# Kernel tuning notes

Measured on AMD Instinct MI355X. Metric: run time of the kernel, lower is better.

The kernel has to match this reference:

```python
import jax, jax.numpy as jnp
import numpy as np

N_NODES = 100000
N_EDGES = 1600000
IN_DIM = 128
HID = 128
NUM_LAYERS = 10
NUM_CLASSES = 2
NUM_GRAPHS = 64


def setup_inputs() -> dict:
    key = jax.random.key(0)
    ks = jax.random.split(key, 16)
    x = jax.random.normal(ks[0], (N_NODES, IN_DIM), dtype=jnp.float32)
    # edges with no self loops (GIN_Conv calls remove_self_loops)
    src = jax.random.randint(ks[1], (N_EDGES,), 0, N_NODES)
    off = jax.random.randint(ks[2], (N_EDGES,), 1, N_NODES)
    dst = (src + off) % N_NODES
    edge_index = jnp.stack([src, dst]).astype(jnp.int64)
    batch = jnp.sort(jax.random.randint(ks[3], (N_NODES,), 0, NUM_GRAPHS)).astype(jnp.int64)
    s = 1.0 / np.sqrt(HID)
    eps = jnp.zeros((NUM_LAYERS,), dtype=jnp.float32)
    W1 = jax.random.normal(ks[4], (NUM_LAYERS, IN_DIM, HID), dtype=jnp.float32) * s
    b1 = jnp.zeros((NUM_LAYERS, HID), dtype=jnp.float32)
    W2 = jax.random.normal(ks[5], (NUM_LAYERS, HID, HID), dtype=jnp.float32) * s
    b2 = jnp.zeros((NUM_LAYERS, HID), dtype=jnp.float32)
    Wc1 = jax.random.normal(ks[6], (HID, HID), dtype=jnp.float32) * s
    bc1 = jnp.zeros((HID,), dtype=jnp.float32)
    Wc2 = jax.random.normal(ks[7], (HID, NUM_CLASSES), dtype=jnp.float32) * s
    bc2 = jnp.zeros((NUM_CLASSES,), dtype=jnp.float32)
    return {"x": x, "edge_index": edge_index, "batch": batch, "eps": eps,
            "W1": W1, "b1": b1, "W2": W2, "b2": b2,
            "Wc1": Wc1, "bc1": bc1, "Wc2": Wc2, "bc2": bc2}


def _gin_block(x, src, dst, eps_i, W1_i, b1_i, W2_i, b2_i, mlp_residual):
    # gather-scatter add aggregation: aggr[v] = sum_{(u->v)} x[u]
    aggr = jax.ops.segment_sum(x[src], dst, num_segments=N_NODES)
    h = (1.0 + eps_i) * x + aggr
    out = jnp.dot(jax.nn.relu(jnp.dot(h, W1_i) + b1_i), W2_i) + b2_i
    if mlp_residual:  # MLP internal residual (layers i > 0)
        out = out + h
    out = jax.nn.relu(out)  # ResidualGNNBlock: Identity norm, relu, Identity dropout
    out = out + x  # block residual (dims match: in_dim == hidden)
    return out


def reference(x, edge_index, batch, eps, W1, b1, W2, b2, Wc1, bc1, Wc2, bc2):
    src, dst = edge_index[0], edge_index[1]
    for i in range(NUM_LAYERS):
        x = _gin_block(x, src, dst, eps[i], W1[i], b1[i], W2[i], b2[i], mlp_residual=(i > 0))
    # global_mean_pool
    sums = jax.ops.segment_sum(x, batch, num_segments=NUM_GRAPHS)
    cnts = jax.ops.segment_sum(jnp.ones((x.shape[0], 1), x.dtype), batch, num_segments=NUM_GRAPHS)
    pooled = sums / jnp.maximum(cnts, 1.0)
    # classifier MLP (dropout inactive in eval)
    logits = jnp.dot(jax.nn.relu(jnp.dot(pooled, Wc1) + bc1), Wc2) + bc2
    return logits
```

## Files before the change

kernel.cpp:

```cpp
#include <hip/hip_runtime.h>


#define N_NODES 100000
#define N_EDGES 1600000
#define HID 128
#define NUM_LAYERS 10
#define NUM_GRAPHS 64
#define SCAN_BLOCKS ((N_NODES + 255) / 256)
#define ROWS 32
#define IDX_CAP 1024


__global__ __launch_bounds__(256) void count_deg_kernel(const int* __restrict__ dst,
                                                        int* __restrict__ deg, int E) {
  int e = blockIdx.x * 256 + threadIdx.x;
  if (e < E) atomicAdd(&deg[dst[e]], 1);
}

__global__ __launch_bounds__(256) void block_sum_kernel(const int* __restrict__ deg,
                                                        int* __restrict__ psum, int n) {
  __shared__ int sd[256];
  int i = blockIdx.x * 256 + threadIdx.x;
  sd[threadIdx.x] = (i < n) ? deg[i] : 0;
  __syncthreads();
  for (int off = 128; off > 0; off >>= 1) {
    if (threadIdx.x < off) sd[threadIdx.x] += sd[threadIdx.x + off];
    __syncthreads();
  }
  if (threadIdx.x == 0) psum[blockIdx.x] = sd[0];
}

__global__ __launch_bounds__(512) void scan_partials_kernel(const int* __restrict__ psum,
                                                            int* __restrict__ poff, int nb) {
  __shared__ int sd[512];
  int i = threadIdx.x;
  int v = (i < nb) ? psum[i] : 0;
  sd[i] = v;
  __syncthreads();
  for (int off = 1; off < 512; off <<= 1) {
    int t = (i >= off) ? sd[i - off] : 0;
    __syncthreads();
    sd[i] += t;
    __syncthreads();
  }
  if (i < nb) poff[i] = sd[i] - v;
}

__global__ __launch_bounds__(256) void write_rs_kernel(const int* __restrict__ deg,
                                                       const int* __restrict__ poff,
                                                       int* __restrict__ rs,
                                                       int* __restrict__ cur, int n) {
  __shared__ int sd[256];
  int i = blockIdx.x * 256 + threadIdx.x;
  int v = (i < n) ? deg[i] : 0;
  sd[threadIdx.x] = v;
  __syncthreads();
  for (int off = 1; off < 256; off <<= 1) {
    int t = (threadIdx.x >= off) ? sd[threadIdx.x - off] : 0;
    __syncthreads();
    sd[threadIdx.x] += t;
    __syncthreads();
  }
  if (i < n) {
    int incl = poff[blockIdx.x] + sd[threadIdx.x];
    rs[i + 1] = incl;
    cur[i] = incl - v;
  }
  if (i == 0) rs[0] = 0;
}

__global__ __launch_bounds__(256) void fill_csr_kernel(const int* __restrict__ src,
                                                       const int* __restrict__ dst,
                                                       int* __restrict__ cur,
                                                       int* __restrict__ csr, int E) {
  int e = blockIdx.x * 256 + threadIdx.x;
  if (e < E) {
    int p = atomicAdd(&cur[dst[e]], 1);
    csr[p] = src[e];
  }
}


__global__ __launch_bounds__(256, 6) void layer_kernel(const float* __restrict__ xin,
                                                       float* __restrict__ xout,
                                                       const int* __restrict__ rs,
                                                       const int* __restrict__ csr,
                                                       const float* __restrict__ eps, int layer,
                                                       const float* __restrict__ W1,
                                                       const float* __restrict__ b1,
                                                       const float* __restrict__ W2,
                                                       const float* __restrict__ b2,
                                                       int n, int addH) {
  __shared__ float lh[ROWS * 128];
  __shared__ int lidx[IDX_CAP];
  const int tid = threadIdx.x;
  const int row0 = blockIdx.x * ROWS;
  const float4* x4 = (const float4*)xin;
  float4* lh4 = (float4*)lh;
  const float s = 1.0f + eps[layer];

  int rowEnd = row0 + ROWS; if (rowEnd > n) rowEnd = n;
  const int eBase = rs[row0];
  const int cnt = rs[rowEnd] - eBase;
  const int stage = (cnt < IDX_CAP) ? cnt : IDX_CAP;
  for (int t = tid; t < stage; t += 256) lidx[t] = csr[eBase + t];
  __syncthreads();

  const int w = tid >> 5;
  const int lane = tid & 31;
#pragma unroll
  for (int it = 0; it < ROWS / 8; ++it) {
    int li = it * 8 + w;
    int node = row0 + li;
    float ax = 0.f, ay = 0.f, az = 0.f, aw = 0.f;
    if (node < n) {
      float4 v = x4[node * 32 + lane];
      ax = v.x * s; ay = v.y * s; az = v.z * s; aw = v.w * s;
      const int e0 = rs[node];
      const int m = rs[node + 1] - e0;
      const int lb = e0 - eBase;
      int i = 0;
      if (lb + m <= stage) {
        for (; i + 8 <= m; i += 8) {
          int u0 = lidx[lb + i + 0], u1 = lidx[lb + i + 1];
          int u2 = lidx[lb + i + 2], u3 = lidx[lb + i + 3];
          int u4 = lidx[lb + i + 4], u5 = lidx[lb + i + 5];
          int u6 = lidx[lb + i + 6], u7 = lidx[lb + i + 7];
          float4 t0 = x4[u0 * 32 + lane];
          float4 t1 = x4[u1 * 32 + lane];
          float4 t2 = x4[u2 * 32 + lane];
          float4 t3 = x4[u3 * 32 + lane];
          float4 t4 = x4[u4 * 32 + lane];
          float4 t5 = x4[u5 * 32 + lane];
          float4 t6 = x4[u6 * 32 + lane];
          float4 t7 = x4[u7 * 32 + lane];
          ax += t0.x + t1.x + t2.x + t3.x + t4.x + t5.x + t6.x + t7.x;
          ay += t0.y + t1.y + t2.y + t3.y + t4.y + t5.y + t6.y + t7.y;
          az += t0.z + t1.z + t2.z + t3.z + t4.z + t5.z + t6.z + t7.z;
          aw += t0.w + t1.w + t2.w + t3.w + t4.w + t5.w + t6.w + t7.w;
        }
        if (i + 4 <= m) {
          int u0 = lidx[lb + i + 0], u1 = lidx[lb + i + 1];
          int u2 = lidx[lb + i + 2], u3 = lidx[lb + i + 3];
          float4 t0 = x4[u0 * 32 + lane];
          float4 t1 = x4[u1 * 32 + lane];
          float4 t2 = x4[u2 * 32 + lane];
          float4 t3 = x4[u3 * 32 + lane];
          ax += t0.x + t1.x + t2.x + t3.x;
          ay += t0.y + t1.y + t2.y + t3.y;
          az += t0.z + t1.z + t2.z + t3.z;
          aw += t0.w + t1.w + t2.w + t3.w;
          i += 4;
        }
        if (i + 2 <= m) {
          int u0 = lidx[lb + i + 0], u1 = lidx[lb + i + 1];
          float4 t0 = x4[u0 * 32 + lane];
          float4 t1 = x4[u1 * 32 + lane];
          ax += t0.x + t1.x; ay += t0.y + t1.y;
          az += t0.z + t1.z; aw += t0.w + t1.w;
          i += 2;
        }
        if (i < m) {
          int u = lidx[lb + i];
          float4 t = x4[u * 32 + lane];
          ax += t.x; ay += t.y; az += t.z; aw += t.w;
        }
      } else {
        for (; i < m; ++i) {
          int u = csr[e0 + i];
          float4 t = x4[u * 32 + lane];
          ax += t.x; ay += t.y; az += t.z; aw += t.w;
        }
      }
    }
    float4 r; r.x = ax; r.y = ay; r.z = az; r.w = aw;
    lh4[li * 32 + lane] = r;
  }
  __syncthreads();

  const int cg = tid & 31;
  const int rg = tid >> 5;
  float acc[4][4];
#pragma unroll
  for (int r = 0; r < 4; ++r) { acc[r][0] = acc[r][1] = acc[r][2] = acc[r][3] = 0.f; }

  for (int k4 = 0; k4 < 32; ++k4) {
    float4 w0 = *(const float4*)(W1 + (k4 * 4 + 0) * 128 + cg * 4);
    float4 w1 = *(const float4*)(W1 + (k4 * 4 + 1) * 128 + cg * 4);
    float4 w2 = *(const float4*)(W1 + (k4 * 4 + 2) * 128 + cg * 4);
    float4 w3 = *(const float4*)(W1 + (k4 * 4 + 3) * 128 + cg * 4);
#pragma unroll
    for (int r = 0; r < 4; ++r) {
      float4 a = *(const float4*)(lh + (rg * 4 + r) * 128 + k4 * 4);
      acc[r][0] += a.x * w0.x + a.y * w1.x + a.z * w2.x + a.w * w3.x;
      acc[r][1] += a.x * w0.y + a.y * w1.y + a.z * w2.y + a.w * w3.y;
      acc[r][2] += a.x * w0.z + a.y * w1.z + a.z * w2.z + a.w * w3.z;
      acc[r][3] += a.x * w0.w + a.y * w1.w + a.z * w2.w + a.w * w3.w;
    }
  }

  float4 hreg[4];
#pragma unroll
  for (int r = 0; r < 4; ++r) hreg[r] = *(const float4*)(lh + (rg * 4 + r) * 128 + cg * 4);
  __syncthreads();

  {
    float4 bb = *(const float4*)(b1 + cg * 4);
#pragma unroll
    for (int r = 0; r < 4; ++r) {
      float4 o;
      o.x = fmaxf(acc[r][0] + bb.x, 0.f);
      o.y = fmaxf(acc[r][1] + bb.y, 0.f);
      o.z = fmaxf(acc[r][2] + bb.z, 0.f);
      o.w = fmaxf(acc[r][3] + bb.w, 0.f);
      *(float4*)(lh + (rg * 4 + r) * 128 + cg * 4) = o;
      acc[r][0] = acc[r][1] = acc[r][2] = acc[r][3] = 0.f;
    }
  }
  __syncthreads();

  for (int k4 = 0; k4 < 32; ++k4) {
    float4 w0 = *(const float4*)(W2 + (k4 * 4 + 0) * 128 + cg * 4);
    float4 w1 = *(const float4*)(W2 + (k4 * 4 + 1) * 128 + cg * 4);
    float4 w2 = *(const float4*)(W2 + (k4 * 4 + 2) * 128 + cg * 4);
    float4 w3 = *(const float4*)(W2 + (k4 * 4 + 3) * 128 + cg * 4);
#pragma unroll
    for (int r = 0; r < 4; ++r) {
      float4 a = *(const float4*)(lh + (rg * 4 + r) * 128 + k4 * 4);
      acc[r][0] += a.x * w0.x + a.y * w1.x + a.z * w2.x + a.w * w3.x;
      acc[r][1] += a.x * w0.y + a.y * w1.y + a.z * w2.y + a.w * w3.y;
      acc[r][2] += a.x * w0.z + a.y * w1.z + a.z * w2.z + a.w * w3.z;
      acc[r][3] += a.x * w0.w + a.y * w1.w + a.z * w2.w + a.w * w3.w;
    }
  }

  float4 b2v = *(const float4*)(b2 + cg * 4);
  float4* xo4 = (float4*)xout;
#pragma unroll
  for (int r = 0; r < 4; ++r) {
    int row = row0 + rg * 4 + r;
    if (row < n) {
      float ox = acc[r][0] + b2v.x;
      float oy = acc[r][1] + b2v.y;
      float oz = acc[r][2] + b2v.z;
      float ow = acc[r][3] + b2v.w;
      if (addH) {
        ox += hreg[r].x; oy += hreg[r].y; oz += hreg[r].z; ow += hreg[r].w;
      }
      ox = fmaxf(ox, 0.f); oy = fmaxf(oy, 0.f); oz = fmaxf(oz, 0.f); ow = fmaxf(ow, 0.f);
      float4 xv = x4[row * 32 + cg];
      float4 o;
      o.x = ox + xv.x; o.y = oy + xv.y; o.z = oz + xv.z; o.w = ow + xv.w;
      xo4[row * 32 + cg] = o;
    }
  }
}


__global__ __launch_bounds__(128) void pool_kernel(const float* __restrict__ x,
                                                   const int* __restrict__ batch,
                                                   float* __restrict__ pool,
                                                   int* __restrict__ gcnt, int n) {
  const int CH = 512;
  int c = threadIdx.x;
  int n0 = blockIdx.x * CH;
  if (n0 >= n) return;
  int n1 = n0 + CH; if (n1 > n) n1 = n;
  float acc = 0.f;
  int g = batch[n0];
  int cl = 0;
  for (int i = n0; i < n1; ++i) {
    int gi = batch[i];
    if (gi != g) {
      atomicAdd(&pool[g * 128 + c], acc);
      if (c == 0) atomicAdd(&gcnt[g], cl);
      acc = 0.f; cl = 0; g = gi;
    }
    acc += x[i * 128 + c];
    cl++;
  }
  atomicAdd(&pool[g * 128 + c], acc);
  if (c == 0) atomicAdd(&gcnt[g], cl);
}


__global__ __launch_bounds__(128) void classifier_kernel(const float* __restrict__ pool,
                                                         const int* __restrict__ gcnt,
                                                         const float* __restrict__ Wc1,
                                                         const float* __restrict__ bc1,
                                                         const float* __restrict__ Wc2,
                                                         const float* __restrict__ bc2,
                                                         float* __restrict__ out) {
  __shared__ float prow[128];
  __shared__ float hid[128];
  int g = blockIdx.x;
  int c = threadIdx.x;
  float cf = (float)gcnt[g];
  if (cf < 1.f) cf = 1.f;
  prow[c] = pool[g * 128 + c] / cf;
  __syncthreads();
  float a = bc1[c];
  for (int k = 0; k < 128; ++k) a += prow[k] * Wc1[k * 128 + c];
  hid[c] = fmaxf(a, 0.f);
  __syncthreads();
  if (c < 2) {
    float a2 = bc2[c];
    for (int k = 0; k < 128; ++k) a2 += hid[k] * Wc2[k * 2 + c];
    out[g * 2 + c] = a2;
  }
}


extern "C" void kernel_launch(void* const* d_in, const int* in_sizes, int n_in,
                              void* d_out, int out_size, void* d_ws, size_t ws_size,
                              hipStream_t stream) {
  const float* x_in = (const float*)d_in[0];
  const int* edge_index = (const int*)d_in[1];
  const int* batch = (const int*)d_in[2];
  const float* eps = (const float*)d_in[3];
  const float* W1 = (const float*)d_in[4];
  const float* b1 = (const float*)d_in[5];
  const float* W2 = (const float*)d_in[6];
  const float* b2 = (const float*)d_in[7];
  const float* Wc1 = (const float*)d_in[8];
  const float* bc1 = (const float*)d_in[9];
  const float* Wc2 = (const float*)d_in[10];
  const float* bc2 = (const float*)d_in[11];
  float* out = (float*)d_out;

  const int N = N_NODES, E = N_EDGES;
  const int* src = edge_index;
  const int* dst = edge_index + E;

  float* xa = (float*)d_ws;
  float* xb = xa + (size_t)N * 128;
  int* deg = (int*)(xb + (size_t)N * 128);
  int* rs = deg + N;
  int* cur = rs + (N + 1);
  int* csr = cur + N;
  float* pool = (float*)(csr + E);
  int* gcnt = (int*)(pool + NUM_GRAPHS * 128);
  int* psum = gcnt + NUM_GRAPHS;
  int* poff = psum + SCAN_BLOCKS;

  hipMemsetAsync(deg, 0, N * sizeof(int), stream);

  count_deg_kernel<<<(E + 255) / 256, 256, 0, stream>>>(dst, deg, E);
  block_sum_kernel<<<SCAN_BLOCKS, 256, 0, stream>>>(deg, psum, N);
  scan_partials_kernel<<<1, 512, 0, stream>>>(psum, poff, SCAN_BLOCKS);
  write_rs_kernel<<<SCAN_BLOCKS, 256, 0, stream>>>(deg, poff, rs, cur, N);
  fill_csr_kernel<<<(E + 255) / 256, 256, 0, stream>>>(src, dst, cur, csr, E);

  for (int i = 0; i < NUM_LAYERS; ++i) {
    const float* xi = (i == 0) ? x_in : ((i % 2 == 0) ? xb : xa);
    float* xo = (i % 2 == 0) ? xa : xb;
    layer_kernel<<<(N + ROWS - 1) / ROWS, 256, 0, stream>>>(xi, xo, rs, csr, eps, i,
                                                    W1 + (size_t)i * 128 * 128, b1 + (size_t)i * 128,
                                                    W2 + (size_t)i * 128 * 128, b2 + (size_t)i * 128,
                                                    N, i > 0 ? 1 : 0);
  }
  const float* xfin = (NUM_LAYERS % 2 == 0) ? xb : xa;

  hipMemsetAsync(pool, 0, NUM_GRAPHS * 128 * sizeof(float), stream);
  hipMemsetAsync(gcnt, 0, NUM_GRAPHS * sizeof(int), stream);
  pool_kernel<<<(N + 511) / 512, 128, 0, stream>>>(xfin, batch, pool, gcnt, N);
  classifier_kernel<<<NUM_GRAPHS, 128, 0, stream>>>(pool, gcnt, Wc1, bc1, Wc2, bc2, out);
}
```

Baseline: 2.501 ms.

## Split fused layer kernel into separate aggregation and MLP kernels

Splits the per-layer fused gather-plus-MLP kernel into an aggregation kernel that writes h to a global buffer and an MLP kernel that reads it back. The aggregation kernel drops the large shared tile so it can run at higher occupancy (launch bounds 8), which may help the latency-bound gather. The cost is an extra global write and read of h per layer plus an extra launch. The MLP kernel reads xres and writes xout into the same buffer (xa) in place; this is safe only if each block reads and writes just its own rows.

```diff
diff --git a/kernel.cpp b/kernel.cpp
--- a/kernel.cpp
+++ b/kernel.cpp
@@ -81,22 +81,17 @@
 }
 
 
-__global__ __launch_bounds__(256, 6) void layer_kernel(const float* __restrict__ xin,
-                                                       float* __restrict__ xout,
-                                                       const int* __restrict__ rs,
-                                                       const int* __restrict__ csr,
-                                                       const float* __restrict__ eps, int layer,
-                                                       const float* __restrict__ W1,
-                                                       const float* __restrict__ b1,
-                                                       const float* __restrict__ W2,
-                                                       const float* __restrict__ b2,
-                                                       int n, int addH) {
-  __shared__ float lh[ROWS * 128];
+__global__ __launch_bounds__(256, 8) void aggr_kernel(const float* __restrict__ xin,
+                                                      float* __restrict__ h,
+                                                      const int* __restrict__ rs,
+                                                      const int* __restrict__ csr,
+                                                      const float* __restrict__ eps, int layer,
+                                                      int n) {
   __shared__ int lidx[IDX_CAP];
   const int tid = threadIdx.x;
   const int row0 = blockIdx.x * ROWS;
   const float4* x4 = (const float4*)xin;
-  float4* lh4 = (float4*)lh;
+  float4* h4 = (float4*)h;
   const float s = 1.0f + eps[layer];
 
   int rowEnd = row0 + ROWS; if (rowEnd > n) rowEnd = n;
@@ -172,9 +167,30 @@
           ax += t.x; ay += t.y; az += t.z; aw += t.w;
         }
       }
-    }
-    float4 r; r.x = ax; r.y = ay; r.z = az; r.w = aw;
-    lh4[li * 32 + lane] = r;
+      float4 r; r.x = ax; r.y = ay; r.z = az; r.w = aw;
+      h4[node * 32 + lane] = r;
+    }
+  }
+}
+
+
+__global__ __launch_bounds__(256, 6) void mlp_kernel(const float* __restrict__ hbuf,
+                                                     const float* __restrict__ xres,
+                                                     float* __restrict__ xout,
+                                                     const float* __restrict__ W1,
+                                                     const float* __restrict__ b1,
+                                                     const float* __restrict__ W2,
+                                                     const float* __restrict__ b2,
+                                                     int n, int addH) {
+  __shared__ float lh[ROWS * 128];
+  const int tid = threadIdx.x;
+  const int row0 = blockIdx.x * ROWS;
+  const float4* h4 = (const float4*)hbuf;
+  const float4* x4 = (const float4*)xres;
+  float4* lh4 = (float4*)lh;
+
+  for (int t = tid; t < ROWS * 32; t += 256) {
+    lh4[t] = h4[(size_t)row0 * 32 + t];
   }
   __syncthreads();
 
@@ -333,8 +349,8 @@
   const int* dst = edge_index + E;
 
   float* xa = (float*)d_ws;
-  float* xb = xa + (size_t)N * 128;
-  int* deg = (int*)(xb + (size_t)N * 128);
+  float* hbuf = xa + (size_t)N * 128;
+  int* deg = (int*)(hbuf + (size_t)N * 128);
   int* rs = deg + N;
   int* cur = rs + (N + 1);
   int* csr = cur + N;
@@ -351,18 +367,18 @@
   write_rs_kernel<<<SCAN_BLOCKS, 256, 0, stream>>>(deg, poff, rs, cur, N);
   fill_csr_kernel<<<(E + 255) / 256, 256, 0, stream>>>(src, dst, cur, csr, E);
 
+  const int NB = (N + ROWS - 1) / ROWS;
   for (int i = 0; i < NUM_LAYERS; ++i) {
-    const float* xi = (i == 0) ? x_in : ((i % 2 == 0) ? xb : xa);
-    float* xo = (i % 2 == 0) ? xa : xb;
-    layer_kernel<<<(N + ROWS - 1) / ROWS, 256, 0, stream>>>(xi, xo, rs, csr, eps, i,
-                                                    W1 + (size_t)i * 128 * 128, b1 + (size_t)i * 128,
-                                                    W2 + (size_t)i * 128 * 128, b2 + (size_t)i * 128,
-                                                    N, i > 0 ? 1 : 0);
-  }
-  const float* xfin = (NUM_LAYERS % 2 == 0) ? xb : xa;
+    const float* xi = (i == 0) ? x_in : xa;
+    aggr_kernel<<<NB, 256, 0, stream>>>(xi, hbuf, rs, csr, eps, i, N);
+    mlp_kernel<<<NB, 256, 0, stream>>>(hbuf, xi, xa,
+                                       W1 + (size_t)i * 128 * 128, b1 + (size_t)i * 128,
+                                       W2 + (size_t)i * 128 * 128, b2 + (size_t)i * 128,
+                                       N, i > 0 ? 1 : 0);
+  }
 
   hipMemsetAsync(pool, 0, NUM_GRAPHS * 128 * sizeof(float), stream);
   hipMemsetAsync(gcnt, 0, NUM_GRAPHS * sizeof(int), stream);
-  pool_kernel<<<(N + 511) / 512, 128, 0, stream>>>(xfin, batch, pool, gcnt, N);
+  pool_kernel<<<(N + 511) / 512, 128, 0, stream>>>(xa, batch, pool, gcnt, N);
   classifier_kernel<<<NUM_GRAPHS, 128, 0, stream>>>(pool, gcnt, Wc1, bc1, Wc2, bc2, out);
 }
```

Result: slower. 3.076 ms (+23.0%).

## Gather neighbor features from a bf16 shadow copy of node features

Applied to the files above, without the earlier changes.

Keeps a bf16 copy of the node features, written by each layer's epilogue and by an initial cast kernel, and does the 16-neighbor gather-sum from that copy. Each gathered row is half as many bytes, which targets the memory-bound aggregation. The fp32 features are now updated in place in one buffer, because each block reads only its own fp32 rows and writes them back. The trade is lost precision in the aggregation that compounds over 10 layers, plus an extra bf16 write per layer.

```diff
diff --git a/kernel.cpp b/kernel.cpp
--- a/kernel.cpp
+++ b/kernel.cpp
@@ -10,6 +10,17 @@
 #define ROWS 32
 #define IDX_CAP 1024
 
+typedef unsigned short ushort_t;
+
+__device__ __forceinline__ float bf2f(unsigned short v) {
+  return __uint_as_float(((unsigned)v) << 16);
+}
+__device__ __forceinline__ unsigned short f2bf(float f) {
+  unsigned u = __float_as_uint(f);
+  unsigned r = u + 0x7FFFu + ((u >> 16) & 1u);
+  return (unsigned short)(r >> 16);
+}
+
 
 __global__ __launch_bounds__(256) void count_deg_kernel(const int* __restrict__ dst,
                                                         int* __restrict__ deg, int E) {
@@ -80,9 +91,22 @@
   }
 }
 
+__global__ __launch_bounds__(256) void cast_bf16_kernel(const float* __restrict__ xin,
+                                                        ushort_t* __restrict__ xh, int n4) {
+  int i = blockIdx.x * 256 + threadIdx.x;
+  if (i < n4) {
+    float4 v = ((const float4*)xin)[i];
+    ushort4 o;
+    o.x = f2bf(v.x); o.y = f2bf(v.y); o.z = f2bf(v.z); o.w = f2bf(v.w);
+    ((ushort4*)xh)[i] = o;
+  }
+}
+
 
 __global__ __launch_bounds__(256, 6) void layer_kernel(const float* __restrict__ xin,
                                                        float* __restrict__ xout,
+                                                       const ushort_t* __restrict__ xh_in,
+                                                       ushort_t* __restrict__ xh_out,
                                                        const int* __restrict__ rs,
                                                        const int* __restrict__ csr,
                                                        const float* __restrict__ eps, int layer,
@@ -96,6 +120,7 @@
   const int tid = threadIdx.x;
   const int row0 = blockIdx.x * ROWS;
   const float4* x4 = (const float4*)xin;
+  const ushort4* xh4 = (const ushort4*)xh_in;
   float4* lh4 = (float4*)lh;
   const float s = 1.0f + eps[layer];
 
@@ -126,50 +151,54 @@
           int u2 = lidx[lb + i + 2], u3 = lidx[lb + i + 3];
           int u4 = lidx[lb + i + 4], u5 = lidx[lb + i + 5];
           int u6 = lidx[lb + i + 6], u7 = lidx[lb + i + 7];
-          float4 t0 = x4[u0 * 32 + lane];
-          float4 t1 = x4[u1 * 32 + lane];
-          float4 t2 = x4[u2 * 32 + lane];
-          float4 t3 = x4[u3 * 32 + lane];
-          float4 t4 = x4[u4 * 32 + lane];
-          float4 t5 = x4[u5 * 32 + lane];
-          float4 t6 = x4[u6 * 32 + lane];
-          float4 t7 = x4[u7 * 32 + lane];
-          ax += t0.x + t1.x + t2.x + t3.x + t4.x + t5.x + t6.x + t7.x;
-          ay += t0.y + t1.y + t2.y + t3.y + t4.y + t5.y + t6.y + t7.y;
-          az += t0.z + t1.z + t2.z + t3.z + t4.z + t5.z + t6.z + t7.z;
-          aw += t0.w + t1.w + t2.w + t3.w + t4.w + t5.w + t6.w + t7.w;
+          ushort4 t0 = xh4[u0 * 32 + lane];
+          ushort4 t1 = xh4[u1 * 32 + lane];
+          ushort4 t2 = xh4[u2 * 32 + lane];
+          ushort4 t3 = xh4[u3 * 32 + lane];
+          ushort4 t4 = xh4[u4 * 32 + lane];
+          ushort4 t5 = xh4[u5 * 32 + lane];
+          ushort4 t6 = xh4[u6 * 32 + lane];
+          ushort4 t7 = xh4[u7 * 32 + lane];
+          ax += bf2f(t0.x) + bf2f(t1.x) + bf2f(t2.x) + bf2f(t3.x)
+              + bf2f(t4.x) + bf2f(t5.x) + bf2f(t6.x) + bf2f(t7.x);
+          ay += bf2f(t0.y) + bf2f(t1.y) + bf2f(t2.y) + bf2f(t3.y)
+              + bf2f(t4.y) + bf2f(t5.y) + bf2f(t6.y) + bf2f(t7.y);
+          az += bf2f(t0.z) + bf2f(t1.z) + bf2f(t2.z) + bf2f(t3.z)
+              + bf2f(t4.z) + bf2f(t5.z) + bf2f(t6.z) + bf2f(t7.z);
+          aw += bf2f(t0.w) + bf2f(t1.w) + bf2f(t2.w) + bf2f(t3.w)
+              + bf2f(t4.w) + bf2f(t5.w) + bf2f(t6.w) + bf2f(t7.w);
         }
         if (i + 4 <= m) {
           int u0 = lidx[lb + i + 0], u1 = lidx[lb + i + 1];
           int u2 = lidx[lb + i + 2], u3 = lidx[lb + i + 3];
-          float4 t0 = x4[u0 * 32 + lane];
-          float4 t1 = x4[u1 * 32 + lane];
-          float4 t2 = x4[u2 * 32 + lane];
-          float4 t3 = x4[u3 * 32 + lane];
-          ax += t0.x + t1.x + t2.x + t3.x;
-          ay += t0.y + t1.y + t2.y + t3.y;
-          az += t0.z + t1.z + t2.z + t3.z;
-          aw += t0.w + t1.w + t2.w + t3.w;
+          ushort4 t0 = xh4[u0 * 32 + lane];
+          ushort4 t1 = xh4[u1 * 32 + lane];
+          ushort4 t2 = xh4[u2 * 32 + lane];
+          ushort4 t3 = xh4[u3 * 32 + lane];
+          ax += bf2f(t0.x) + bf2f(t1.x) + bf2f(t2.x) + bf2f(t3.x);
+          ay += bf2f(t0.y) + bf2f(t1.y) + bf2f(t2.y) + bf2f(t3.y);
+          az += bf2f(t0.z) + bf2f(t1.z) + bf2f(t2.z) + bf2f(t3.z);
+          aw += bf2f(t0.w) + bf2f(t1.w) + bf2f(t2.w) + bf2f(t3.w);
           i += 4;
         }
         if (i + 2 <= m) {
           int u0 = lidx[lb + i + 0], u1 = lidx[lb + i + 1];
-          float4 t0 = x4[u0 * 32 + lane];
-          float4 t1 = x4[u1 * 32 + lane];
-          ax += t0.x + t1.x; ay += t0.y + t1.y;
-          az += t0.z + t1.z; aw += t0.w + t1.w;
+          ushort4 t0 = xh4[u0 * 32 + lane];
+          ushort4 t1 = xh4[u1 * 32 + lane];
+          ax += bf2f(t0.x) + bf2f(t1.x); ay += bf2f(t0.y) + bf2f(t1.y);
+          az += bf2f(t0.z) + bf2f(t1.z); aw += bf2f(t0.w) + bf2f(t1.w);
           i += 2;
         }
         if (i < m) {
           int u = lidx[lb + i];
-          float4 t = x4[u * 32 + lane];
-          ax += t.x; ay += t.y; az += t.z; aw += t.w;
+          ushort4 t = xh4[u * 32 + lane];
+          ax += bf2f(t.x); ay += bf2f(t.y); az += bf2f(t.z); aw += bf2f(t.w);
         }
       } else {
         for (; i < m; ++i) {
           int u = csr[e0 + i];
-          float4 t = x4[u * 32 + lane];
-          ax += t.x; ay += t.y; az += t.z; aw += t.w;
+          ushort4 t = xh4[u * 32 + lane];
+          ax += bf2f(t.x); ay += bf2f(t.y); az += bf2f(t.z); aw += bf2f(t.w);
         }
       }
     }
@@ -236,6 +265,7 @@
 
   float4 b2v = *(const float4*)(b2 + cg * 4);
   float4* xo4 = (float4*)xout;
+  ushort4* xho4 = (ushort4*)xh_out;
 #pragma unroll
   for (int r = 0; r < 4; ++r) {
     int row = row0 + rg * 4 + r;
@@ -252,6 +282,9 @@
       float4 o;
       o.x = ox + xv.x; o.y = oy + xv.y; o.z = oz + xv.z; o.w = ow + xv.w;
       xo4[row * 32 + cg] = o;
+      ushort4 ob;
+      ob.x = f2bf(o.x); ob.y = f2bf(o.y); ob.z = f2bf(o.z); ob.w = f2bf(o.w);
+      xho4[row * 32 + cg] = ob;
     }
   }
 }
@@ -333,8 +366,9 @@
   const int* dst = edge_index + E;
 
   float* xa = (float*)d_ws;
-  float* xb = xa + (size_t)N * 128;
-  int* deg = (int*)(xb + (size_t)N * 128);
+  ushort_t* xha = (ushort_t*)(xa + (size_t)N * 128);
+  ushort_t* xhb = xha + (size_t)N * 128;
+  int* deg = (int*)(xhb + (size_t)N * 128);
   int* rs = deg + N;
   int* cur = rs + (N + 1);
   int* csr = cur + N;
@@ -351,18 +385,21 @@
   write_rs_kernel<<<SCAN_BLOCKS, 256, 0, stream>>>(deg, poff, rs, cur, N);
   fill_csr_kernel<<<(E + 255) / 256, 256, 0, stream>>>(src, dst, cur, csr, E);
 
+  cast_bf16_kernel<<<(N * 32 + 255) / 256, 256, 0, stream>>>(x_in, xha, N * 32);
+
+  const int NB = (N + ROWS - 1) / ROWS;
   for (int i = 0; i < NUM_LAYERS; ++i) {
-    const float* xi = (i == 0) ? x_in : ((i % 2 == 0) ? xb : xa);
-    float* xo = (i % 2 == 0) ? xa : xb;
-    layer_kernel<<<(N + ROWS - 1) / ROWS, 256, 0, stream>>>(xi, xo, rs, csr, eps, i,
-                                                    W1 + (size_t)i * 128 * 128, b1 + (size_t)i * 128,
-                                                    W2 + (size_t)i * 128 * 128, b2 + (size_t)i * 128,
-                                                    N, i > 0 ? 1 : 0);
-  }
-  const float* xfin = (NUM_LAYERS % 2 == 0) ? xb : xa;
+    const float* xi = (i == 0) ? x_in : xa;
+    const ushort_t* gin = (i % 2 == 0) ? xha : xhb;
+    ushort_t* gout = (i % 2 == 0) ? xhb : xha;
+    layer_kernel<<<NB, 256, 0, stream>>>(xi, xa, gin, gout, rs, csr, eps, i,
+                                         W1 + (size_t)i * 128 * 128, b1 + (size_t)i * 128,
+                                         W2 + (size_t)i * 128 * 128, b2 + (size_t)i * 128,
+                                         N, i > 0 ? 1 : 0);
+  }
 
   hipMemsetAsync(pool, 0, NUM_GRAPHS * 128 * sizeof(float), stream);
   hipMemsetAsync(gcnt, 0, NUM_GRAPHS * sizeof(int), stream);
-  pool_kernel<<<(N + 511) / 512, 128, 0, stream>>>(xfin, batch, pool, gcnt, N);
+  pool_kernel<<<(N + 511) / 512, 128, 0, stream>>>(xa, batch, pool, gcnt, N);
   classifier_kernel<<<NUM_GRAPHS, 128, 0, stream>>>(pool, gcnt, Wc1, bc1, Wc2, bc2, out);
 }
```

New measurement: 2.301 ms. 1.09x faster.
